# Optimization experiments

Hardware: AMD Instinct MI355X
Metric: run time of the kernel (lower is better)

The kernel has to match this reference:

```python
import jax, jax.numpy as jnp
import numpy as np

B, S, D, H = 2, 2048, 1024, 16
DK = D // H


def setup_inputs() -> dict:
    key = jax.random.key(0)
    ks = jax.random.split(key, 11)
    scale = 1.0 / np.sqrt(D)
    inp = {
        "q": jax.random.normal(ks[0], (B, S, D), jnp.float32),
        "k": jax.random.normal(ks[1], (B, S, D), jnp.float32),
        "v": jax.random.normal(ks[2], (B, S, D), jnp.float32),
        # causal mask, broadcastable to (B, H, S, S); 0 = masked
        "mask": jnp.tril(jnp.ones((S, S), jnp.int32))[None, None, :, :],
        "wq": jax.random.normal(ks[3], (D, D), jnp.float32) * scale,
        "bq": jax.random.normal(ks[4], (D,), jnp.float32) * scale,
        "wk": jax.random.normal(ks[5], (D, D), jnp.float32) * scale,
        "bk": jax.random.normal(ks[6], (D,), jnp.float32) * scale,
        "wv": jax.random.normal(ks[7], (D, D), jnp.float32) * scale,
        "bv": jax.random.normal(ks[8], (D,), jnp.float32) * scale,
        "wo": jax.random.normal(ks[9], (D, D), jnp.float32) * scale,
        "bo": jax.random.normal(ks[10], (D,), jnp.float32) * scale,
    }
    return inp


def reference(q, k, v, mask, wq, bq, wk, bk, wv, bv, wo, bo):
    # Linear projections (torch Linear: y = x @ W^T + b)
    Q = jnp.einsum('bsd,ed->bse', q, wq) + bq
    K = jnp.einsum('bsd,ed->bse', k, wk) + bk
    V = jnp.einsum('bsd,ed->bse', v, wv) + bv
    # split heads -> (B, H, S, d_k)
    Q = Q.reshape(B, S, H, DK).transpose(0, 2, 1, 3)
    K = K.reshape(B, S, H, DK).transpose(0, 2, 1, 3)
    V = V.reshape(B, S, H, DK).transpose(0, 2, 1, 3)
    # naive full-score attention, faithful to the source
    scores = jnp.einsum('bhqd,bhkd->bhqk', Q, K) / jnp.sqrt(jnp.float32(DK))
    scores = jnp.where(mask == 0, -jnp.inf, scores)
    attn = jax.nn.softmax(scores, axis=-1)
    out = jnp.einsum('bhqk,bhkd->bhqd', attn, V)
    # merge heads -> (B, S, D)
    out = out.transpose(0, 2, 1, 3).reshape(B, S, D)
    return jnp.einsum('bsd,ed->bse', out, wo) + bo
```

## Files before the change

### kernel.cpp

```cpp
#include <hip/hip_runtime.h>
#include <hip/hip_bf16.h>
#include <cstdint>

constexpr int Bc = 2, Sc = 2048, Dc = 1024, Hc = 16;
constexpr int Mtok = Bc * Sc;

typedef __bf16 bf16;
typedef __bf16 bf16x8 __attribute__((ext_vector_type(8)));
typedef float  f32x4  __attribute__((ext_vector_type(4)));

__global__ __launch_bounds__(256) void convert_all(
    const float* __restrict__ q, const float* __restrict__ k,
    const float* __restrict__ v, const float* __restrict__ wq,
    const float* __restrict__ wk, const float* __restrict__ wv,
    const float* __restrict__ wo, bf16* __restrict__ ws)
{
  constexpr size_t NQ = (size_t)Mtok * Dc;
  constexpr size_t NW = (size_t)Dc * Dc;
  const size_t e = ((size_t)blockIdx.x * 256 + threadIdx.x) * 8;
  const float* src; bf16* dst;
  if (e < 3 * NQ) {
    src = (e < NQ) ? q + e : (e < 2 * NQ) ? k + (e - NQ) : v + (e - 2 * NQ);
    dst = ws + e;
  } else {
    const size_t w = e - 3 * NQ;
    const float* wsrc = (w < NW) ? wq : (w < 2 * NW) ? wk : (w < 3 * NW) ? wv : wo;
    src = wsrc + (w & (NW - 1));
    dst = ws + 5 * NQ + w;
  }
  f32x4 a = ((const f32x4*)src)[0];
  f32x4 b = ((const f32x4*)src)[1];
  bf16x8 t;
  t[0]=(bf16)a[0]; t[1]=(bf16)a[1]; t[2]=(bf16)a[2]; t[3]=(bf16)a[3];
  t[4]=(bf16)b[0]; t[5]=(bf16)b[1]; t[6]=(bf16)b[2]; t[7]=(bf16)b[3];
  *(bf16x8*)dst = t;
}

template <bool AF32, bool BF32, bool OUTF32>
__global__ __launch_bounds__(256) void gemm128(
    const void* __restrict__ Av, const void* __restrict__ Bv,
    const float* __restrict__ bias, void* __restrict__ Yv,
    int M, int N, int K)
{
  __shared__ __attribute__((aligned(16))) bf16 As[2][128][40];
  __shared__ __attribute__((aligned(16))) bf16 Bs[2][128][40];

  const int m0 = blockIdx.x * 128, n0 = blockIdx.y * 128;
  const int tid = threadIdx.x, wave = tid >> 6, lane = tid & 63;
  const int quad = lane >> 4, l16 = lane & 15;
  const int rw = wave >> 1, cw = wave & 1;
  const int srow = tid >> 1, sc = (tid & 1) * 16;

  f32x4 acc[4][4] = {};

  auto loadA = [&](int k0, bf16x8& lo, bf16x8& hi) {
    if constexpr (AF32) {
      const float* s = (const float*)Av + (size_t)(m0 + srow) * K + k0 + sc;
      f32x4 a0 = ((const f32x4*)s)[0], a1 = ((const f32x4*)s)[1];
      f32x4 a2 = ((const f32x4*)s)[2], a3 = ((const f32x4*)s)[3];
      lo[0]=(bf16)a0[0]; lo[1]=(bf16)a0[1]; lo[2]=(bf16)a0[2]; lo[3]=(bf16)a0[3];
      lo[4]=(bf16)a1[0]; lo[5]=(bf16)a1[1]; lo[6]=(bf16)a1[2]; lo[7]=(bf16)a1[3];
      hi[0]=(bf16)a2[0]; hi[1]=(bf16)a2[1]; hi[2]=(bf16)a2[2]; hi[3]=(bf16)a2[3];
      hi[4]=(bf16)a3[0]; hi[5]=(bf16)a3[1]; hi[6]=(bf16)a3[2]; hi[7]=(bf16)a3[3];
    } else {
      const bf16* s = (const bf16*)Av + (size_t)(m0 + srow) * K + k0 + sc;
      lo = ((const bf16x8*)s)[0]; hi = ((const bf16x8*)s)[1];
    }
  };
  auto loadB = [&](int k0, bf16x8& lo, bf16x8& hi) {
    if constexpr (BF32) {
      const float* s = (const float*)Bv + (size_t)(n0 + srow) * K + k0 + sc;
      f32x4 a0 = ((const f32x4*)s)[0], a1 = ((const f32x4*)s)[1];
      f32x4 a2 = ((const f32x4*)s)[2], a3 = ((const f32x4*)s)[3];
      lo[0]=(bf16)a0[0]; lo[1]=(bf16)a0[1]; lo[2]=(bf16)a0[2]; lo[3]=(bf16)a0[3];
      lo[4]=(bf16)a1[0]; lo[5]=(bf16)a1[1]; lo[6]=(bf16)a1[2]; lo[7]=(bf16)a1[3];
      hi[0]=(bf16)a2[0]; hi[1]=(bf16)a2[1]; hi[2]=(bf16)a2[2]; hi[3]=(bf16)a2[3];
      hi[4]=(bf16)a3[0]; hi[5]=(bf16)a3[1]; hi[6]=(bf16)a3[2]; hi[7]=(bf16)a3[3];
    } else {
      const bf16* s = (const bf16*)Bv + (size_t)(n0 + srow) * K + k0 + sc;
      lo = ((const bf16x8*)s)[0]; hi = ((const bf16x8*)s)[1];
    }
  };

  bf16x8 alo, ahi, blo, bhi;
  loadA(0, alo, ahi); loadB(0, blo, bhi);
  *(bf16x8*)&As[0][srow][sc] = alo; *(bf16x8*)&As[0][srow][sc + 8] = ahi;
  *(bf16x8*)&Bs[0][srow][sc] = blo; *(bf16x8*)&Bs[0][srow][sc + 8] = bhi;

  const int NIT = K >> 5;
  for (int it = 0; it < NIT; ++it) {
    __syncthreads();
    const int cur = it & 1;
    const bool pf = (it + 1) < NIT;
    if (pf) { loadA((it + 1) * 32, alo, ahi); loadB((it + 1) * 32, blo, bhi); }

    bf16x8 af[4];
#pragma unroll
    for (int rt = 0; rt < 4; ++rt)
      af[rt] = *(const bf16x8*)&As[cur][rw * 64 + rt * 16 + l16][quad * 8];
#pragma unroll
    for (int ct = 0; ct < 4; ++ct) {
      bf16x8 bfr = *(const bf16x8*)&Bs[cur][cw * 64 + ct * 16 + l16][quad * 8];
#pragma unroll
      for (int rt = 0; rt < 4; ++rt)
        acc[rt][ct] = __builtin_amdgcn_mfma_f32_16x16x32_bf16(af[rt], bfr, acc[rt][ct], 0, 0, 0);
    }
    if (pf) {
      const int nxt = cur ^ 1;
      *(bf16x8*)&As[nxt][srow][sc] = alo; *(bf16x8*)&As[nxt][srow][sc + 8] = ahi;
      *(bf16x8*)&Bs[nxt][srow][sc] = blo; *(bf16x8*)&Bs[nxt][srow][sc + 8] = bhi;
    }
  }

#pragma unroll
  for (int ct = 0; ct < 4; ++ct) {
    const int col = n0 + cw * 64 + ct * 16 + l16;
    const float bv = bias[col];
#pragma unroll
    for (int rt = 0; rt < 4; ++rt) {
#pragma unroll
      for (int i = 0; i < 4; ++i) {
        const int row = m0 + rw * 64 + rt * 16 + quad * 4 + i;
        const float vv = acc[rt][ct][i] + bv;
        if constexpr (OUTF32) ((float*)Yv)[(size_t)row * N + col] = vv;
        else                  ((bf16*)Yv)[(size_t)row * N + col] = (bf16)vv;
      }
    }
  }
}

__global__ __launch_bounds__(256) void transpose_v(
    const bf16* __restrict__ in, bf16* __restrict__ out)
{
  __shared__ __attribute__((aligned(16))) bf16 tile[64][72];
  const int s0 = blockIdx.x * 64, d0 = blockIdx.y * 64, b = blockIdx.z;
  const int t = threadIdx.x, r = t >> 2, c = (t & 3) * 16;

  const bf16* src = in + (size_t)(b * Sc + s0 + r) * Dc + d0 + c;
  *(bf16x8*)&tile[r][c]     = ((const bf16x8*)src)[0];
  *(bf16x8*)&tile[r][c + 8] = ((const bf16x8*)src)[1];
  __syncthreads();

  bf16x8 t0, t1;
#pragma unroll
  for (int j = 0; j < 8; ++j) t0[j] = tile[c + j][r];
#pragma unroll
  for (int j = 0; j < 8; ++j) t1[j] = tile[c + 8 + j][r];
  bf16* dst = out + (size_t)(b * Dc + d0 + r) * Sc + s0 + c;
  ((bf16x8*)dst)[0] = t0;
  ((bf16x8*)dst)[1] = t1;
}

__global__ __launch_bounds__(256) void attn2(
    const bf16* __restrict__ Q, const bf16* __restrict__ K,
    const bf16* __restrict__ Vt, bf16* __restrict__ O)
{
  __shared__ __attribute__((aligned(16))) bf16 Ks[2][64][72];
  __shared__ __attribute__((aligned(16))) bf16 Vs[2][64][72];
  __shared__ __attribute__((aligned(16))) bf16 Ps[4][16][72];

  const int p = blockIdx.x, h = blockIdx.y, b = blockIdx.z;
  const int tid = threadIdx.x, wave = tid >> 6, lane = tid & 63;
  const int quad = lane >> 4, l16 = lane & 15;
  const int sr = tid >> 2, sc4 = (tid & 3) * 16;

  const bf16 onec = (bf16)1.0f;
  const bf16x8 ones = {onec, onec, onec, onec, onec, onec, onec, onec};

  for (int half = 0; half < 2; ++half) {
    const int tile = half ? (31 - p) : p;
    const int q0 = tile * 64;
    const int nkb = tile + 1;

    const bf16* qrow = Q + (size_t)(b * Sc + q0 + wave * 16 + l16) * Dc + h * 64 + quad * 8;
    const bf16x8 aq0 = *(const bf16x8*)qrow;
    const bf16x8 aq1 = *(const bf16x8*)(qrow + 32);

    f32x4 oacc[4] = {{0,0,0,0},{0,0,0,0},{0,0,0,0},{0,0,0,0}};
    f32x4 lacc = {0, 0, 0, 0};

    __syncthreads();
    {
      const bf16* ksrc = K + (size_t)(b * Sc + sr) * Dc + h * 64 + sc4;
      ((bf16x8*)&Ks[0][sr][sc4])[0] = ((const bf16x8*)ksrc)[0];
      ((bf16x8*)&Ks[0][sr][sc4])[1] = ((const bf16x8*)ksrc)[1];
      const bf16* vsrc = Vt + (size_t)(b * Dc + h * 64 + sr) * Sc + sc4;
      ((bf16x8*)&Vs[0][sr][sc4])[0] = ((const bf16x8*)vsrc)[0];
      ((bf16x8*)&Vs[0][sr][sc4])[1] = ((const bf16x8*)vsrc)[1];
    }

    for (int kb = 0; kb < nkb; ++kb) {
      __syncthreads();
      const int cur = kb & 1;
      const bool pf = (kb + 1) < nkb;
      bf16x8 kp0, kp1, vp0, vp1;
      if (pf) {
        const bf16* ksrc = K + (size_t)(b * Sc + (kb + 1) * 64 + sr) * Dc + h * 64 + sc4;
        kp0 = ((const bf16x8*)ksrc)[0]; kp1 = ((const bf16x8*)ksrc)[1];
        const bf16* vsrc = Vt + (size_t)(b * Dc + h * 64 + sr) * Sc + (kb + 1) * 64 + sc4;
        vp0 = ((const bf16x8*)vsrc)[0]; vp1 = ((const bf16x8*)vsrc)[1];
      }

      f32x4 s[4] = {{0,0,0,0},{0,0,0,0},{0,0,0,0},{0,0,0,0}};
#pragma unroll
      for (int d2 = 0; d2 < 2; ++d2) {
        const bf16x8 a = d2 ? aq1 : aq0;
#pragma unroll
        for (int ct = 0; ct < 4; ++ct) {
          bf16x8 bk = *(const bf16x8*)&Ks[cur][ct * 16 + l16][d2 * 32 + quad * 8];
          s[ct] = __builtin_amdgcn_mfma_f32_16x16x32_bf16(a, bk, s[ct], 0, 0, 0);
        }
      }

      const bool diag = (kb == nkb - 1);
#pragma unroll
      for (int ct = 0; ct < 4; ++ct) {
#pragma unroll
        for (int i = 0; i < 4; ++i) {
          float e = __expf(s[ct][i] * 0.125f);
          if (diag && (ct * 16 + l16 > wave * 16 + quad * 4 + i)) e = 0.f;
          Ps[wave][quad * 4 + i][ct * 16 + l16] = (bf16)e;
        }
      }
      const bf16x8 ap0 = *(const bf16x8*)&Ps[wave][l16][quad * 8];
      const bf16x8 ap1 = *(const bf16x8*)&Ps[wave][l16][32 + quad * 8];

      lacc = __builtin_amdgcn_mfma_f32_16x16x32_bf16(ap0, ones, lacc, 0, 0, 0);
      lacc = __builtin_amdgcn_mfma_f32_16x16x32_bf16(ap1, ones, lacc, 0, 0, 0);

#pragma unroll
      for (int d2 = 0; d2 < 2; ++d2) {
        const bf16x8 ap = d2 ? ap1 : ap0;
#pragma unroll
        for (int ct = 0; ct < 4; ++ct) {
          bf16x8 bv = *(const bf16x8*)&Vs[cur][ct * 16 + l16][d2 * 32 + quad * 8];
          oacc[ct] = __builtin_amdgcn_mfma_f32_16x16x32_bf16(ap, bv, oacc[ct], 0, 0, 0);
        }
      }

      if (pf) {
        const int nxt = cur ^ 1;
        ((bf16x8*)&Ks[nxt][sr][sc4])[0] = kp0; ((bf16x8*)&Ks[nxt][sr][sc4])[1] = kp1;
        ((bf16x8*)&Vs[nxt][sr][sc4])[0] = vp0; ((bf16x8*)&Vs[nxt][sr][sc4])[1] = vp1;
      }
    }

    f32x4 rl;
#pragma unroll
    for (int i = 0; i < 4; ++i) rl[i] = 1.0f / lacc[i];
#pragma unroll
    for (int ct = 0; ct < 4; ++ct)
#pragma unroll
      for (int i = 0; i < 4; ++i)
        O[(size_t)(b * Sc + q0 + wave * 16 + quad * 4 + i) * Dc + h * 64 + ct * 16 + l16] =
            (bf16)(oacc[ct][i] * rl[i]);
  }
}

extern "C" void kernel_launch(void* const* d_in, const int* in_sizes, int n_in,
                              void* d_out, int out_size, void* d_ws, size_t ws_size,
                              hipStream_t stream)
{
  const float* q  = (const float*)d_in[0];
  const float* k  = (const float*)d_in[1];
  const float* v  = (const float*)d_in[2];
  const float* wq = (const float*)d_in[4];
  const float* bq = (const float*)d_in[5];
  const float* wk = (const float*)d_in[6];
  const float* bk = (const float*)d_in[7];
  const float* wv = (const float*)d_in[8];
  const float* bv = (const float*)d_in[9];
  const float* wo = (const float*)d_in[10];
  const float* bo = (const float*)d_in[11];
  float* out = (float*)d_out;

  constexpr size_t NQ = (size_t)Mtok * Dc;
  constexpr size_t NW = (size_t)Dc * Dc;
  bf16* W = (bf16*)d_ws;
  const dim3 gg(Mtok / 128, Dc / 128);
  const dim3 ga(16, Hc, Bc);
  const dim3 gt(Sc / 64, Dc / 64, Bc);

  const bool fancy = ws_size >= (size_t)(5 * NQ + 4 * NW) * 2;
  if (fancy) {
    bf16* xq = W;
    bf16* xk = W + NQ;
    bf16* xv = W + 2 * NQ;
    bf16* Qp = W + 3 * NQ;
    bf16* Kp = W + 4 * NQ;
    bf16* wb = W + 5 * NQ;
    bf16* Vp = W;
    bf16* AO = W + NQ;
    bf16* Vt = W + 2 * NQ;

    convert_all<<<8192, 256, 0, stream>>>(q, k, v, wq, wk, wv, wo, W);
    gemm128<false, false, false><<<gg, 256, 0, stream>>>(xq, wb,          bq, Qp, Mtok, Dc, Dc);
    gemm128<false, false, false><<<gg, 256, 0, stream>>>(xk, wb + NW,     bk, Kp, Mtok, Dc, Dc);
    gemm128<false, false, false><<<gg, 256, 0, stream>>>(xv, wb + 2 * NW, bv, Vp, Mtok, Dc, Dc);
    transpose_v<<<gt, 256, 0, stream>>>(Vp, Vt);
    attn2<<<ga, 256, 0, stream>>>(Qp, Kp, Vt, AO);
    gemm128<false, false, true><<<gg, 256, 0, stream>>>(AO, wb + 3 * NW, bo, out, Mtok, Dc, Dc);
  } else {
    bf16* Qp = W;
    bf16* Kp = W + NQ;
    bf16* Vp = W + 2 * NQ;
    bf16* Vt = W + 3 * NQ;
    bf16* AO = W + 4 * NQ;
    gemm128<true, true, false><<<gg, 256, 0, stream>>>(q, wq, bq, Qp, Mtok, Dc, Dc);
    gemm128<true, true, false><<<gg, 256, 0, stream>>>(k, wk, bk, Kp, Mtok, Dc, Dc);
    gemm128<true, true, false><<<gg, 256, 0, stream>>>(v, wv, bv, Vp, Mtok, Dc, Dc);
    transpose_v<<<gt, 256, 0, stream>>>(Vp, Vt);
    attn2<<<ga, 256, 0, stream>>>(Qp, Kp, Vt, AO);
    gemm128<false, true, true><<<gg, 256, 0, stream>>>(AO, wo, bo, out, Mtok, Dc, Dc);
  }
}
```

Measured before the change: 258.7 us.

## Batch QKV GEMMs, use direct global-to-LDS loads, enlarge attention tiles to 128 queries

Merges the three QKV projection GEMMs into one launch over a z grid dimension, and switches both it and a new 64-row output-projection GEMM to global_load_lds transfers. These drop register staging but also drop double buffering, so each k-step waits on two barriers. The attention kernel now uses 512 threads with 128-query tiles, which halves K/V reloads per query and changes the grid to 8 tile pairs per batch-head. Causal masking now applies to the last two key blocks. The cost is less overlap of loads with compute and fewer attention blocks.

```diff
diff --git a/kernel.cpp b/kernel.cpp
--- a/kernel.cpp
+++ b/kernel.cpp
@@ -8,6 +8,12 @@
 typedef __bf16 bf16;
 typedef __bf16 bf16x8 __attribute__((ext_vector_type(8)));
 typedef float  f32x4  __attribute__((ext_vector_type(4)));
+
+__device__ __forceinline__ void gld_lds16(const bf16* g, bf16* l) {
+  __builtin_amdgcn_global_load_lds(
+      (__attribute__((address_space(1))) void*)(void*)g,
+      (__attribute__((address_space(3))) void*)l, 16, 0, 0);
+}
 
 __global__ __launch_bounds__(256) void convert_all(
     const float* __restrict__ q, const float* __restrict__ k,
@@ -36,6 +42,118 @@
   *(bf16x8*)dst = t;
 }
 
+__global__ __launch_bounds__(256) void gemm_qkv(
+    const bf16* __restrict__ Aq, const bf16* __restrict__ Ak,
+    const bf16* __restrict__ Av, const bf16* __restrict__ Wb,
+    const float* __restrict__ bq, const float* __restrict__ bk,
+    const float* __restrict__ bv,
+    bf16* __restrict__ Yq, bf16* __restrict__ Yk, bf16* __restrict__ Yv)
+{
+  __shared__ __attribute__((aligned(16))) bf16 As[128 * 32];
+  __shared__ __attribute__((aligned(16))) bf16 Bs[128 * 32];
+
+  const int z = blockIdx.z;
+  const bf16*  A    = (z == 0) ? Aq : (z == 1) ? Ak : Av;
+  const bf16*  Wz   = Wb + (size_t)z * Dc * Dc;
+  const float* bias = (z == 0) ? bq : (z == 1) ? bk : bv;
+  bf16*        Y    = (z == 0) ? Yq : (z == 1) ? Yk : Yv;
+
+  const int m0 = blockIdx.x * 128, n0 = blockIdx.y * 128;
+  const int tid = threadIdx.x, wave = tid >> 6, lane = tid & 63;
+  const int quad = lane >> 4, l16 = lane & 15;
+  const int rw = wave >> 1, cw = wave & 1;
+  const int srow = wave * 16 + (lane >> 2);
+  const int scol = (lane & 3) * 8;
+
+  f32x4 acc[4][4] = {};
+
+  for (int k0 = 0; k0 < Dc; k0 += 32) {
+#pragma unroll
+    for (int s = 0; s < 2; ++s) {
+      const int row = s * 64 + srow;
+      gld_lds16(A  + (size_t)(m0 + row) * Dc + k0 + scol, &As[s * 2048 + wave * 512]);
+      gld_lds16(Wz + (size_t)(n0 + row) * Dc + k0 + scol, &Bs[s * 2048 + wave * 512]);
+    }
+    __syncthreads();
+    bf16x8 af[4];
+#pragma unroll
+    for (int rt = 0; rt < 4; ++rt)
+      af[rt] = *(const bf16x8*)&As[(rw * 64 + rt * 16 + l16) * 32 + quad * 8];
+#pragma unroll
+    for (int ct = 0; ct < 4; ++ct) {
+      bf16x8 bfr = *(const bf16x8*)&Bs[(cw * 64 + ct * 16 + l16) * 32 + quad * 8];
+#pragma unroll
+      for (int rt = 0; rt < 4; ++rt)
+        acc[rt][ct] = __builtin_amdgcn_mfma_f32_16x16x32_bf16(af[rt], bfr, acc[rt][ct], 0, 0, 0);
+    }
+    __syncthreads();
+  }
+
+#pragma unroll
+  for (int ct = 0; ct < 4; ++ct) {
+    const int col = n0 + cw * 64 + ct * 16 + l16;
+    const float bvv = bias[col];
+#pragma unroll
+    for (int rt = 0; rt < 4; ++rt)
+#pragma unroll
+      for (int i = 0; i < 4; ++i) {
+        const int row = m0 + rw * 64 + rt * 16 + quad * 4 + i;
+        Y[(size_t)row * Dc + col] = (bf16)(acc[rt][ct][i] + bvv);
+      }
+  }
+}
+
+__global__ __launch_bounds__(256) void gemm_o(
+    const bf16* __restrict__ A, const bf16* __restrict__ Wz,
+    const float* __restrict__ bias, float* __restrict__ Y)
+{
+  __shared__ __attribute__((aligned(16))) bf16 As[64 * 32];
+  __shared__ __attribute__((aligned(16))) bf16 Bs[128 * 32];
+
+  const int m0 = blockIdx.x * 64, n0 = blockIdx.y * 128;
+  const int tid = threadIdx.x, wave = tid >> 6, lane = tid & 63;
+  const int quad = lane >> 4, l16 = lane & 15;
+  const int srow = wave * 16 + (lane >> 2);
+  const int scol = (lane & 3) * 8;
+
+  f32x4 acc[4][2] = {};
+
+  for (int k0 = 0; k0 < Dc; k0 += 32) {
+    gld_lds16(A + (size_t)(m0 + srow) * Dc + k0 + scol, &As[wave * 512]);
+#pragma unroll
+    for (int s = 0; s < 2; ++s) {
+      const int row = s * 64 + srow;
+      gld_lds16(Wz + (size_t)(n0 + row) * Dc + k0 + scol, &Bs[s * 2048 + wave * 512]);
+    }
+    __syncthreads();
+    bf16x8 af[4];
+#pragma unroll
+    for (int rt = 0; rt < 4; ++rt)
+      af[rt] = *(const bf16x8*)&As[(rt * 16 + l16) * 32 + quad * 8];
+#pragma unroll
+    for (int ct = 0; ct < 2; ++ct) {
+      bf16x8 bfr = *(const bf16x8*)&Bs[(wave * 32 + ct * 16 + l16) * 32 + quad * 8];
+#pragma unroll
+      for (int rt = 0; rt < 4; ++rt)
+        acc[rt][ct] = __builtin_amdgcn_mfma_f32_16x16x32_bf16(af[rt], bfr, acc[rt][ct], 0, 0, 0);
+    }
+    __syncthreads();
+  }
+
+#pragma unroll
+  for (int ct = 0; ct < 2; ++ct) {
+    const int col = n0 + wave * 32 + ct * 16 + l16;
+    const float bvv = bias[col];
+#pragma unroll
+    for (int rt = 0; rt < 4; ++rt)
+#pragma unroll
+      for (int i = 0; i < 4; ++i) {
+        const int row = m0 + rt * 16 + quad * 4 + i;
+        Y[(size_t)row * Dc + col] = acc[rt][ct][i] + bvv;
+      }
+  }
+}
+
 template <bool AF32, bool BF32, bool OUTF32>
 __global__ __launch_bounds__(256) void gemm128(
     const void* __restrict__ Av, const void* __restrict__ Bv,
@@ -53,9 +171,9 @@
 
   f32x4 acc[4][4] = {};
 
-  auto loadA = [&](int k0, bf16x8& lo, bf16x8& hi) {
-    if constexpr (AF32) {
-      const float* s = (const float*)Av + (size_t)(m0 + srow) * K + k0 + sc;
+  auto load = [&](const void* P, bool f32, int r0, int k0, bf16x8& lo, bf16x8& hi) {
+    if (f32) {
+      const float* s = (const float*)P + (size_t)(r0 + srow) * K + k0 + sc;
       f32x4 a0 = ((const f32x4*)s)[0], a1 = ((const f32x4*)s)[1];
       f32x4 a2 = ((const f32x4*)s)[2], a3 = ((const f32x4*)s)[3];
       lo[0]=(bf16)a0[0]; lo[1]=(bf16)a0[1]; lo[2]=(bf16)a0[2]; lo[3]=(bf16)a0[3];
@@ -63,27 +181,13 @@
       hi[0]=(bf16)a2[0]; hi[1]=(bf16)a2[1]; hi[2]=(bf16)a2[2]; hi[3]=(bf16)a2[3];
       hi[4]=(bf16)a3[0]; hi[5]=(bf16)a3[1]; hi[6]=(bf16)a3[2]; hi[7]=(bf16)a3[3];
     } else {
-      const bf16* s = (const bf16*)Av + (size_t)(m0 + srow) * K + k0 + sc;
+      const bf16* s = (const bf16*)P + (size_t)(r0 + srow) * K + k0 + sc;
       lo = ((const bf16x8*)s)[0]; hi = ((const bf16x8*)s)[1];
     }
   };
-  auto loadB = [&](int k0, bf16x8& lo, bf16x8& hi) {
-    if constexpr (BF32) {
-      const float* s = (const float*)Bv + (size_t)(n0 + srow) * K + k0 + sc;
-      f32x4 a0 = ((const f32x4*)s)[0], a1 = ((const f32x4*)s)[1];
-      f32x4 a2 = ((const f32x4*)s)[2], a3 = ((const f32x4*)s)[3];
-      lo[0]=(bf16)a0[0]; lo[1]=(bf16)a0[1]; lo[2]=(bf16)a0[2]; lo[3]=(bf16)a0[3];
-      lo[4]=(bf16)a1[0]; lo[5]=(bf16)a1[1]; lo[6]=(bf16)a1[2]; lo[7]=(bf16)a1[3];
-      hi[0]=(bf16)a2[0]; hi[1]=(bf16)a2[1]; hi[2]=(bf16)a2[2]; hi[3]=(bf16)a2[3];
-      hi[4]=(bf16)a3[0]; hi[5]=(bf16)a3[1]; hi[6]=(bf16)a3[2]; hi[7]=(bf16)a3[3];
-    } else {
-      const bf16* s = (const bf16*)Bv + (size_t)(n0 + srow) * K + k0 + sc;
-      lo = ((const bf16x8*)s)[0]; hi = ((const bf16x8*)s)[1];
-    }
-  };
 
   bf16x8 alo, ahi, blo, bhi;
-  loadA(0, alo, ahi); loadB(0, blo, bhi);
+  load(Av, AF32, m0, 0, alo, ahi); load(Bv, BF32, n0, 0, blo, bhi);
   *(bf16x8*)&As[0][srow][sc] = alo; *(bf16x8*)&As[0][srow][sc + 8] = ahi;
   *(bf16x8*)&Bs[0][srow][sc] = blo; *(bf16x8*)&Bs[0][srow][sc + 8] = bhi;
 
@@ -92,7 +196,7 @@
     __syncthreads();
     const int cur = it & 1;
     const bool pf = (it + 1) < NIT;
-    if (pf) { loadA((it + 1) * 32, alo, ahi); loadB((it + 1) * 32, blo, bhi); }
+    if (pf) { load(Av, AF32, m0, (it+1)*32, alo, ahi); load(Bv, BF32, n0, (it+1)*32, blo, bhi); }
 
     bf16x8 af[4];
 #pragma unroll
@@ -115,17 +219,16 @@
 #pragma unroll
   for (int ct = 0; ct < 4; ++ct) {
     const int col = n0 + cw * 64 + ct * 16 + l16;
-    const float bv = bias[col];
-#pragma unroll
-    for (int rt = 0; rt < 4; ++rt) {
+    const float bvv = bias[col];
+#pragma unroll
+    for (int rt = 0; rt < 4; ++rt)
 #pragma unroll
       for (int i = 0; i < 4; ++i) {
         const int row = m0 + rw * 64 + rt * 16 + quad * 4 + i;
-        const float vv = acc[rt][ct][i] + bv;
+        const float vv = acc[rt][ct][i] + bvv;
         if constexpr (OUTF32) ((float*)Yv)[(size_t)row * N + col] = vv;
         else                  ((bf16*)Yv)[(size_t)row * N + col] = (bf16)vv;
       }
-    }
   }
 }
 
@@ -151,26 +254,27 @@
   ((bf16x8*)dst)[1] = t1;
 }
 
-__global__ __launch_bounds__(256) void attn2(
+__global__ __launch_bounds__(512) void attn3(
     const bf16* __restrict__ Q, const bf16* __restrict__ K,
     const bf16* __restrict__ Vt, bf16* __restrict__ O)
 {
-  __shared__ __attribute__((aligned(16))) bf16 Ks[2][64][72];
-  __shared__ __attribute__((aligned(16))) bf16 Vs[2][64][72];
-  __shared__ __attribute__((aligned(16))) bf16 Ps[4][16][72];
-
-  const int p = blockIdx.x, h = blockIdx.y, b = blockIdx.z;
+  __shared__ __attribute__((aligned(16))) bf16 Ks[2][64][68];
+  __shared__ __attribute__((aligned(16))) bf16 Vs[2][64][68];
+  __shared__ __attribute__((aligned(16))) bf16 Ps[8][16][68];
+
+  const int bh = blockIdx.x, b = bh >> 4, h = bh & 15;
+  const int pr = blockIdx.y;
   const int tid = threadIdx.x, wave = tid >> 6, lane = tid & 63;
   const int quad = lane >> 4, l16 = lane & 15;
-  const int sr = tid >> 2, sc4 = (tid & 3) * 16;
+  const int sr = tid >> 3, sc8 = (tid & 7) * 8;
 
   const bf16 onec = (bf16)1.0f;
   const bf16x8 ones = {onec, onec, onec, onec, onec, onec, onec, onec};
 
   for (int half = 0; half < 2; ++half) {
-    const int tile = half ? (31 - p) : p;
-    const int q0 = tile * 64;
-    const int nkb = tile + 1;
+    const int qt = half ? (15 - pr) : pr;
+    const int q0 = qt * 128;
+    const int nkb = 2 * (qt + 1);
 
     const bf16* qrow = Q + (size_t)(b * Sc + q0 + wave * 16 + l16) * Dc + h * 64 + quad * 8;
     const bf16x8 aq0 = *(const bf16x8*)qrow;
@@ -180,25 +284,17 @@
     f32x4 lacc = {0, 0, 0, 0};
 
     __syncthreads();
-    {
-      const bf16* ksrc = K + (size_t)(b * Sc + sr) * Dc + h * 64 + sc4;
-      ((bf16x8*)&Ks[0][sr][sc4])[0] = ((const bf16x8*)ksrc)[0];
-      ((bf16x8*)&Ks[0][sr][sc4])[1] = ((const bf16x8*)ksrc)[1];
-      const bf16* vsrc = Vt + (size_t)(b * Dc + h * 64 + sr) * Sc + sc4;
-      ((bf16x8*)&Vs[0][sr][sc4])[0] = ((const bf16x8*)vsrc)[0];
-      ((bf16x8*)&Vs[0][sr][sc4])[1] = ((const bf16x8*)vsrc)[1];
-    }
+    *(bf16x8*)&Ks[0][sr][sc8] = *(const bf16x8*)(K  + (size_t)(b * Sc + sr) * Dc + h * 64 + sc8);
+    *(bf16x8*)&Vs[0][sr][sc8] = *(const bf16x8*)(Vt + (size_t)(b * Dc + h * 64 + sr) * Sc + sc8);
 
     for (int kb = 0; kb < nkb; ++kb) {
       __syncthreads();
       const int cur = kb & 1;
       const bool pf = (kb + 1) < nkb;
-      bf16x8 kp0, kp1, vp0, vp1;
+      bf16x8 kp, vp;
       if (pf) {
-        const bf16* ksrc = K + (size_t)(b * Sc + (kb + 1) * 64 + sr) * Dc + h * 64 + sc4;
-        kp0 = ((const bf16x8*)ksrc)[0]; kp1 = ((const bf16x8*)ksrc)[1];
-        const bf16* vsrc = Vt + (size_t)(b * Dc + h * 64 + sr) * Sc + (kb + 1) * 64 + sc4;
-        vp0 = ((const bf16x8*)vsrc)[0]; vp1 = ((const bf16x8*)vsrc)[1];
+        kp = *(const bf16x8*)(K  + (size_t)(b * Sc + (kb + 1) * 64 + sr) * Dc + h * 64 + sc8);
+        vp = *(const bf16x8*)(Vt + (size_t)(b * Dc + h * 64 + sr) * Sc + (kb + 1) * 64 + sc8);
       }
 
       f32x4 s[4] = {{0,0,0,0},{0,0,0,0},{0,0,0,0},{0,0,0,0}};
@@ -212,16 +308,25 @@
         }
       }
 
-      const bool diag = (kb == nkb - 1);
-#pragma unroll
-      for (int ct = 0; ct < 4; ++ct) {
-#pragma unroll
-        for (int i = 0; i < 4; ++i) {
-          float e = __expf(s[ct][i] * 0.125f);
-          if (diag && (ct * 16 + l16 > wave * 16 + quad * 4 + i)) e = 0.f;
-          Ps[wave][quad * 4 + i][ct * 16 + l16] = (bf16)e;
+      if (kb >= nkb - 2) {
+        const int row = q0 + wave * 16 + quad * 4;
+#pragma unroll
+        for (int ct = 0; ct < 4; ++ct) {
+          const int col = kb * 64 + ct * 16 + l16;
+#pragma unroll
+          for (int i = 0; i < 4; ++i) {
+            const float e = (col > row + i) ? 0.f : __expf(s[ct][i] * 0.125f);
+            Ps[wave][quad * 4 + i][ct * 16 + l16] = (bf16)e;
+          }
         }
-      }
+      } else {
+#pragma unroll
+        for (int ct = 0; ct < 4; ++ct)
+#pragma unroll
+          for (int i = 0; i < 4; ++i)
+            Ps[wave][quad * 4 + i][ct * 16 + l16] = (bf16)__expf(s[ct][i] * 0.125f);
+      }
+
       const bf16x8 ap0 = *(const bf16x8*)&Ps[wave][l16][quad * 8];
       const bf16x8 ap1 = *(const bf16x8*)&Ps[wave][l16][32 + quad * 8];
 
@@ -240,8 +345,8 @@
 
       if (pf) {
         const int nxt = cur ^ 1;
-        ((bf16x8*)&Ks[nxt][sr][sc4])[0] = kp0; ((bf16x8*)&Ks[nxt][sr][sc4])[1] = kp1;
-        ((bf16x8*)&Vs[nxt][sr][sc4])[0] = vp0; ((bf16x8*)&Vs[nxt][sr][sc4])[1] = vp1;
+        *(bf16x8*)&Ks[nxt][sr][sc8] = kp;
+        *(bf16x8*)&Vs[nxt][sr][sc8] = vp;
       }
     }
 
@@ -277,8 +382,7 @@
   constexpr size_t NQ = (size_t)Mtok * Dc;
   constexpr size_t NW = (size_t)Dc * Dc;
   bf16* W = (bf16*)d_ws;
-  const dim3 gg(Mtok / 128, Dc / 128);
-  const dim3 ga(16, Hc, Bc);
+  const dim3 ga(Hc * Bc, 8);
   const dim3 gt(Sc / 64, Dc / 64, Bc);
 
   const bool fancy = ws_size >= (size_t)(5 * NQ + 4 * NW) * 2;
@@ -294,23 +398,23 @@
     bf16* Vt = W + 2 * NQ;
 
     convert_all<<<8192, 256, 0, stream>>>(q, k, v, wq, wk, wv, wo, W);
-    gemm128<false, false, false><<<gg, 256, 0, stream>>>(xq, wb,          bq, Qp, Mtok, Dc, Dc);
-    gemm128<false, false, false><<<gg, 256, 0, stream>>>(xk, wb + NW,     bk, Kp, Mtok, Dc, Dc);
-    gemm128<false, false, false><<<gg, 256, 0, stream>>>(xv, wb + 2 * NW, bv, Vp, Mtok, Dc, Dc);
+    gemm_qkv<<<dim3(Mtok / 128, Dc / 128, 3), 256, 0, stream>>>(
+        xq, xk, xv, wb, bq, bk, bv, Qp, Kp, Vp);
     transpose_v<<<gt, 256, 0, stream>>>(Vp, Vt);
-    attn2<<<ga, 256, 0, stream>>>(Qp, Kp, Vt, AO);
-    gemm128<false, false, true><<<gg, 256, 0, stream>>>(AO, wb + 3 * NW, bo, out, Mtok, Dc, Dc);
+    attn3<<<ga, 512, 0, stream>>>(Qp, Kp, Vt, AO);
+    gemm_o<<<dim3(Mtok / 64, Dc / 128), 256, 0, stream>>>(AO, wb + 3 * NW, bo, out);
   } else {
     bf16* Qp = W;
     bf16* Kp = W + NQ;
     bf16* Vp = W + 2 * NQ;
     bf16* Vt = W + 3 * NQ;
     bf16* AO = W + 4 * NQ;
+    const dim3 gg(Mtok / 128, Dc / 128);
     gemm128<true, true, false><<<gg, 256, 0, stream>>>(q, wq, bq, Qp, Mtok, Dc, Dc);
     gemm128<true, true, false><<<gg, 256, 0, stream>>>(k, wk, bk, Kp, Mtok, Dc, Dc);
     gemm128<true, true, false><<<gg, 256, 0, stream>>>(v, wv, bv, Vp, Mtok, Dc, Dc);
     transpose_v<<<gt, 256, 0, stream>>>(Vp, Vt);
-    attn2<<<ga, 256, 0, stream>>>(Qp, Kp, Vt, AO);
+    attn3<<<ga, 512, 0, stream>>>(Qp, Kp, Vt, AO);
     gemm128<false, true, true><<<gg, 256, 0, stream>>>(AO, wo, bo, out, Mtok, Dc, Dc);
   }
 }
```

After: 236.5 us. 1.09x faster.
